# Kernel optimization log

Measured on AMD Instinct MI355X. Metric: run time of the kernel, lower is better.

Reference implementation:

```python
import jax, jax.numpy as jnp
import numpy as np

B, C, H, W = 2, 256, 64, 64
FEAT = 256          # in_channels * expansion_ratio
HEADS = 8
HS = FEAT // HEADS  # 32
OUT = 256


def setup_inputs() -> dict:
    key = jax.random.key(0)
    ks = jax.random.split(key, 12)
    inp = {
        "x": jax.random.normal(ks[0], (B, C, H, W), jnp.float32),
        "mod_multiplier": jax.random.normal(ks[1], (B, FEAT), jnp.float32),
        "mod_bias": jax.random.normal(ks[2], (B, FEAT), jnp.float32),
        # learned parameters (1x1 convs as matrices)
        "w_qkv": jax.random.normal(ks[3], (3 * FEAT, C), jnp.float32) * 0.02,
        "b_qkv": jnp.zeros((3 * FEAT,), jnp.float32),
        "w_proj": jax.random.normal(ks[4], (OUT, FEAT), jnp.float32) * 0.02,
        "pe_q_h": jax.random.normal(ks[5], (1, FEAT, H, 1), jnp.float32) * 0.02,
        "pe_q_w": jax.random.normal(ks[6], (1, FEAT, 1, W), jnp.float32) * 0.02,
        "pe_k_h": jax.random.normal(ks[7], (1, FEAT, H, 1), jnp.float32) * 0.02,
        "pe_k_w": jax.random.normal(ks[8], (1, FEAT, 1, W), jnp.float32) * 0.02,
        "pre_act_bias": jnp.zeros((1, C, 1, 1), jnp.float32),
        "pre_qkv_bias": jnp.zeros((1, C, 1, 1), jnp.float32),
        "pre_proj_bias": jnp.zeros((1, FEAT, 1, 1), jnp.float32),
        "id_scale": jnp.ones((1, OUT, 1, 1), jnp.float32),
    }
    return inp


def reference(x, mod_multiplier, mod_bias, w_qkv, b_qkv, w_proj,
              pe_q_h, pe_q_w, pe_k_h, pe_k_w,
              pre_act_bias, pre_qkv_bias, pre_proj_bias, id_scale):
    b = x.shape[0]
    # pre-activation (Fixup-style biases)
    x_preact = jax.nn.silu(x + pre_act_bias) + pre_qkv_bias
    # 1x1 conv -> QKV: [b, 3F, H, W]
    qkv = jnp.einsum('bchw,oc->bohw', x_preact, w_qkv) + b_qkv[None, :, None, None]
    q, k, v = jnp.split(qkv, 3, axis=1)
    # additive positional embeddings
    q = q + pe_q_h + pe_q_w
    k = k + pe_k_h + pe_k_w
    # FiLM modulation of query
    q = q * mod_multiplier[:, :, None, None] + mod_bias[:, :, None, None]
    # [b, heads, head_size, H*W]
    q = q.reshape(b, HEADS, HS, H * W)
    k = k.reshape(b, HEADS, HS, H * W)
    v = v.reshape(b, HEADS, HS, H * W)
    scale = jnp.asarray(HS ** 0.5, x.dtype)
    logits = jnp.einsum('bhdn,bhdm->bhnm', q, k) / scale
    weights = jax.nn.softmax(logits, axis=-1)
    attn = jnp.einsum('bhnm,bhdm->bhdn', weights, v)
    attn = attn.reshape(b, FEAT, H, W)
    # output projection (1x1 conv, no bias)
    x_res = jnp.einsum('bchw,oc->bohw', attn + pre_proj_bias, w_proj)
    return x * id_scale + x_res
```

## Files before the change

### kernel.cpp

```cpp
#include <hip/hip_runtime.h>
#include <hip/hip_bf16.h>
#include <cstdint>

#define NB   2
#define NC   256
#define NN   4096
#define NH   8
#define HSZ  32
#define NF   256
#define N3F  768

typedef __bf16 bf16x8 __attribute__((ext_vector_type(8)));
typedef __bf16 bf16x4 __attribute__((ext_vector_type(4)));
typedef short  s16x4  __attribute__((ext_vector_type(4)));
typedef float  floatx4 __attribute__((ext_vector_type(4)));

#define QSCALE 0.25506601622184f

__global__ void k_prep(const float* __restrict__ x, const float* __restrict__ pab,
                       const float* __restrict__ pqb, __bf16* __restrict__ y,
                       const float* __restrict__ wqkv, const float* __restrict__ wproj,
                       __bf16* __restrict__ wqb, __bf16* __restrict__ wpb) {
    __shared__ __bf16 ct[32 * 264];
    int bid = blockIdx.x, tid = threadIdx.x;
    if (bid >= 256) {
        int id = (bid - 256) * 1024 + tid * 4;
        const float* src = (id < 196608) ? (wqkv + id) : (wproj + (id - 196608));
        __bf16* dst = (id < 196608) ? (wqb + id) : (wpb + (id - 196608));
        float4 v = *(const float4*)src;
        bf16x4 o;
        o[0] = (__bf16)v.x; o[1] = (__bf16)v.y; o[2] = (__bf16)v.z; o[3] = (__bf16)v.w;
        *(bf16x4*)dst = o;
        return;
    }
    int b = bid >> 7, nt = bid & 127;
    int n0 = nt * 32;
    int cbase = tid >> 3, nc = tid & 7;
#pragma unroll
    for (int q = 0; q < 8; q++) {
        int c = cbase + q * 32;
        const float4 xv = *(const float4*)(x + ((size_t)b * NC + c) * NN + n0 + nc * 4);
        float bias = pab[c], qb = pqb[c];
        float vs[4] = {xv.x, xv.y, xv.z, xv.w};
#pragma unroll
        for (int i = 0; i < 4; i++) {
            float s = vs[i] + bias;
            float r = s / (1.f + __expf(-s)) + qb;
            ct[(nc * 4 + i) * 264 + c] = (__bf16)r;
        }
    }
    __syncthreads();
#pragma unroll
    for (int q = 0; q < 4; q++) {
        int id = tid + q * 256;
        int n = id >> 5, ck = (id & 31) * 8;
        bf16x8 v = *(const bf16x8*)(ct + n * 264 + ck);
        *(bf16x8*)(y + ((size_t)b * NN + n0 + n) * NC + ck) = v;
    }
}

__launch_bounds__(256)
__global__ void k_qkv(const __bf16* __restrict__ y, const __bf16* __restrict__ wb,
                      const float* __restrict__ bqkv,
                      const float* __restrict__ peqh, const float* __restrict__ peqw,
                      const float* __restrict__ pekh, const float* __restrict__ pekw,
                      const float* __restrict__ mm, const float* __restrict__ mb,
                      __bf16* __restrict__ qs, __bf16* __restrict__ kst, __bf16* __restrict__ vdm) {
    __shared__ __bf16 smem[4 * 5120];
    __bf16* at0 = smem;
    __bf16* bt0 = smem + 2 * 5120;
    __bf16* ct  = smem;
    const int nt = blockIdx.x, ot = blockIdx.y, b = blockIdx.z;
    const int tid = threadIdx.x;
    const int wave = tid >> 6, lane = tid & 63, ln = lane & 15, quad = lane >> 4;
    const int wm = (wave & 1) * 64, wn = (wave >> 1) * 64;
    floatx4 acc[4][4];
#pragma unroll
    for (int i = 0; i < 4; i++)
#pragma unroll
        for (int j = 0; j < 4; j++) acc[i][j] = 0.f;
    const __bf16* ysrc = y + ((size_t)b * NN + nt * 128) * NC;
    const __bf16* wsrc = wb + (size_t)ot * 128 * NC;
    const int r0 = tid >> 2, c0 = (tid & 3) * 8;
    const int r1 = (tid + 256) >> 2, c1 = ((tid + 256) & 3) * 8;
    bf16x8 ya0, ya1, wa0, wa1;
    ya0 = *(const bf16x8*)(ysrc + (size_t)r0 * NC + c0);
    ya1 = *(const bf16x8*)(ysrc + (size_t)r1 * NC + c1);
    wa0 = *(const bf16x8*)(wsrc + (size_t)r0 * NC + c0);
    wa1 = *(const bf16x8*)(wsrc + (size_t)r1 * NC + c1);
    for (int ko = 0; ko < 8; ko++) {
        int buf = ko & 1;
        *(bf16x8*)(at0 + buf * 5120 + r0 * 40 + c0) = ya0;
        *(bf16x8*)(at0 + buf * 5120 + r1 * 40 + c1) = ya1;
        *(bf16x8*)(bt0 + buf * 5120 + r0 * 40 + c0) = wa0;
        *(bf16x8*)(bt0 + buf * 5120 + r1 * 40 + c1) = wa1;
        __syncthreads();
        if (ko < 7) {
            int kc = (ko + 1) * 32;
            ya0 = *(const bf16x8*)(ysrc + (size_t)r0 * NC + kc + c0);
            ya1 = *(const bf16x8*)(ysrc + (size_t)r1 * NC + kc + c1);
            wa0 = *(const bf16x8*)(wsrc + (size_t)r0 * NC + kc + c0);
            wa1 = *(const bf16x8*)(wsrc + (size_t)r1 * NC + kc + c1);
        }
        const __bf16* atb = at0 + buf * 5120;
        const __bf16* btb = bt0 + buf * 5120;
        bf16x8 af[4], bfr[4];
#pragma unroll
        for (int ii = 0; ii < 4; ii++) af[ii]  = *(const bf16x8*)(atb + (wm + ii * 16 + ln) * 40 + quad * 8);
#pragma unroll
        for (int jj = 0; jj < 4; jj++) bfr[jj] = *(const bf16x8*)(btb + (wn + jj * 16 + ln) * 40 + quad * 8);
#pragma unroll
        for (int ii = 0; ii < 4; ii++)
#pragma unroll
            for (int jj = 0; jj < 4; jj++)
                acc[ii][jj] = __builtin_amdgcn_mfma_f32_16x16x32_bf16(af[ii], bfr[jj], acc[ii][jj], 0, 0, 0);
    }
    __syncthreads();
    if (ot < 4) {
#pragma unroll
        for (int ii = 0; ii < 4; ii++)
#pragma unroll
            for (int jj = 0; jj < 4; jj++) {
                int o_l = wn + jj * 16 + ln;
                int o_g = ot * 128 + o_l;
#pragma unroll
                for (int r = 0; r < 4; r++) {
                    int n_l = wm + ii * 16 + quad * 4 + r;
                    int n_g = nt * 128 + n_l;
                    int hp = n_g >> 6, wp = n_g & 63;
                    float val = acc[ii][jj][r] + bqkv[o_g];
                    if (ot < 2) {
                        val += peqh[o_g * 64 + hp] + peqw[o_g * 64 + wp];
                        val = val * mm[b * NF + o_g] + mb[b * NF + o_g];
                        val *= QSCALE;
                    } else {
                        int c = o_g - 256;
                        val += pekh[c * 64 + hp] + pekw[c * 64 + wp];
                    }
                    ct[n_l * 136 + o_l] = (__bf16)val;
                }
            }
        __syncthreads();
#pragma unroll
        for (int q = 0; q < 8; q++) {
            int id = tid + q * 256;
            int n_l = id >> 4, oc = (id & 15) * 8;
            bf16x8 v = *(const bf16x8*)(ct + n_l * 136 + oc);
            int n_g = nt * 128 + n_l;
            int o_g = ot * 128 + oc;
            if (ot < 2) {
                int h = o_g >> 5, d = o_g & 31;
                *(bf16x8*)(qs + (((size_t)b * NH + h) * NN + n_g) * HSZ + d) = v;
            } else {
                int c = o_g - 256, h = c >> 5, d = c & 31;
                *(bf16x8*)(kst + (((size_t)b * NH + h) * NN + n_g) * HSZ + d) = v;
            }
        }
    } else {
#pragma unroll
        for (int ii = 0; ii < 4; ii++)
#pragma unroll
            for (int jj = 0; jj < 4; jj++) {
                int o_l = wn + jj * 16 + ln;
                int o_g = ot * 128 + o_l;
#pragma unroll
                for (int r = 0; r < 4; r++) {
                    int n_l = wm + ii * 16 + quad * 4 + r;
                    float val = acc[ii][jj][r] + bqkv[o_g];
                    ct[o_l * 136 + n_l] = (__bf16)val;
                }
            }
        __syncthreads();
#pragma unroll
        for (int q = 0; q < 8; q++) {
            int id = tid + q * 256;
            int o_l = id >> 4, ncnk = (id & 15) * 8;
            bf16x8 v = *(const bf16x8*)(ct + o_l * 136 + ncnk);
            int c = ot * 128 + o_l - 512, h = c >> 5, d = c & 31;
            *(bf16x8*)(vdm + (((size_t)b * NH + h) * HSZ + d) * NN + nt * 128 + ncnk) = v;
        }
    }
}

__launch_bounds__(256)
__global__ void k_attn(const __bf16* __restrict__ qs, const __bf16* __restrict__ ksrc,
                       const __bf16* __restrict__ vdm,
                       __bf16* __restrict__ po, float* __restrict__ pl) {
    __shared__ __bf16 kt[2][128 * 40];
    __shared__ __bf16 vt[2][32 * 136];
    int bi = blockIdx.x;
    int xcd = bi & 7, r = bi >> 3;
    int bh = xcd * 2 + (r & 1);
    int r2 = r >> 1;
    int qt = r2 & 31, half = r2 >> 5;
    int m_base = half * 2048;
    int tid = threadIdx.x, wave = tid >> 6, lane = tid & 63, ln = lane & 15, quad = lane >> 4;
    int n0 = qt * 128 + wave * 32;
    const __bf16* qbase = qs + (size_t)bh * NN * HSZ;
    const __bf16* kbase = ksrc + (size_t)bh * NN * HSZ;
    const __bf16* vbase = vdm + (size_t)bh * HSZ * NN;
    bf16x8 qa[2];
    qa[0] = *(const bf16x8*)(qbase + (size_t)(n0 + ln) * HSZ + quad * 8);
    qa[1] = *(const bf16x8*)(qbase + (size_t)(n0 + 16 + ln) * HSZ + quad * 8);
    floatx4 o[2][2];
    o[0][0] = 0.f; o[0][1] = 0.f; o[1][0] = 0.f; o[1][1] = 0.f;
    floatx4 lsum4[2];
    lsum4[0] = 0.f; lsum4[1] = 0.f;
    floatx4 zf = 0.f;
    const int k0r = tid >> 2, k0c = (tid & 3) * 8;
    const int k1r = (tid + 256) >> 2, k1c = ((tid + 256) & 3) * 8;
    const int v0d = tid >> 4, v0m = (tid & 15) * 8;
    const int v1d = (tid + 256) >> 4, v1m = ((tid + 256) & 15) * 8;
    bf16x8 krg0, krg1, vrg0, vrg1;
    krg0 = *(const bf16x8*)(kbase + (size_t)(m_base + k0r) * HSZ + k0c);
    krg1 = *(const bf16x8*)(kbase + (size_t)(m_base + k1r) * HSZ + k1c);
    vrg0 = *(const bf16x8*)(vbase + (size_t)v0d * NN + m_base + v0m);
    vrg1 = *(const bf16x8*)(vbase + (size_t)v1d * NN + m_base + v1m);

    for (int mt = 0; mt < 16; mt++) {
        int buf = mt & 1;
        *(bf16x8*)(&kt[buf][k0r * 40 + k0c]) = krg0;
        *(bf16x8*)(&kt[buf][k1r * 40 + k1c]) = krg1;
        *(bf16x8*)(&vt[buf][v0d * 136 + v0m]) = vrg0;
        *(bf16x8*)(&vt[buf][v1d * 136 + v1m]) = vrg1;
        __syncthreads();
        if (mt < 15) {
            int m1 = m_base + (mt + 1) * 128;
            krg0 = *(const bf16x8*)(kbase + (size_t)(m1 + k0r) * HSZ + k0c);
            krg1 = *(const bf16x8*)(kbase + (size_t)(m1 + k1r) * HSZ + k1c);
            vrg0 = *(const bf16x8*)(vbase + (size_t)v0d * NN + m1 + v0m);
            vrg1 = *(const bf16x8*)(vbase + (size_t)v1d * NN + m1 + v1m);
        }
        const __bf16* ktb = &kt[buf][0];
        const __bf16* vtb = &vt[buf][0];
#pragma unroll
        for (int j = 0; j < 8; j++) {
            bf16x8 kb = *(const bf16x8*)(ktb + (j * 16 + ln) * 40 + quad * 8);
            s16x4 vb0, vb1;
            __builtin_memcpy(&vb0, vtb + ln * 136 + j * 16 + quad * 4, 8);
            __builtin_memcpy(&vb1, vtb + (16 + ln) * 136 + j * 16 + quad * 4, 8);
#pragma unroll
            for (int i = 0; i < 2; i++) {
                floatx4 s = __builtin_amdgcn_mfma_f32_16x16x32_bf16(kb, qa[i], zf, 0, 0, 0);
                bf16x4 p;
#pragma unroll
                for (int rr = 0; rr < 4; rr++) {
                    float e = __builtin_amdgcn_exp2f(s[rr]);
                    lsum4[i][rr] += e;
                    p[rr] = (__bf16)e;
                }
                s16x4 pa;
                __builtin_memcpy(&pa, &p, 8);
                o[i][0] = __builtin_amdgcn_mfma_f32_16x16x16bf16_1k(pa, vb0, o[i][0], 0, 0, 0);
                o[i][1] = __builtin_amdgcn_mfma_f32_16x16x16bf16_1k(pa, vb1, o[i][1], 0, 0, 0);
            }
        }
    }
    size_t pobase = (size_t)(half * 16 + bh) * NN * HSZ;
    size_t plbase = (size_t)(half * 16 + bh) * NN;
#pragma unroll
    for (int i = 0; i < 2; i++) {
        float ls = lsum4[i][0] + lsum4[i][1] + lsum4[i][2] + lsum4[i][3];
        ls += __shfl_xor(ls, 16, 64);
        ls += __shfl_xor(ls, 32, 64);
        if (quad == 0) pl[plbase + n0 + i * 16 + ln] = ls;
#pragma unroll
        for (int rr = 0; rr < 4; rr++) {
            int n_g = n0 + i * 16 + quad * 4 + rr;
#pragma unroll
            for (int dj = 0; dj < 2; dj++)
                po[pobase + (size_t)n_g * HSZ + dj * 16 + ln] = (__bf16)o[i][dj][rr];
        }
    }
}

__launch_bounds__(256)
__global__ void k_proj(const __bf16* __restrict__ po, const float* __restrict__ pl,
                       const __bf16* __restrict__ wpb, const float* __restrict__ ppb,
                       const float* __restrict__ x, const float* __restrict__ idsc,
                       float* __restrict__ out) {
    __shared__ __bf16 at[64 * 264];
    __shared__ __bf16 bt[2][128 * 40];
    __shared__ float linv[8 * 128];
    __shared__ float ppbs[256];
    int nt = blockIdx.x, ot = blockIdx.y, b = blockIdx.z;
    int tid = threadIdx.x, wave = tid >> 6, lane = tid & 63, ln = lane & 15, quad = lane >> 4;
    int wo = (wave & 1) * 32, wn = (wave >> 1) * 64;
#pragma unroll
    for (int q = 0; q < 8; q++) {
        int id = tid + q * 256;
        int row = id >> 5, fc = (id & 31) * 8;
        *(bf16x8*)(at + row * 264 + fc) = *(const bf16x8*)(wpb + (size_t)(ot * 64 + row) * NF + fc);
    }
#pragma unroll
    for (int q = 0; q < 4; q++) {
        int id = tid + q * 256;
        int h = id >> 7, n_l = id & 127;
        size_t base = (size_t)(b * NH + h) * NN + nt * 128 + n_l;
        linv[id] = 1.f / (pl[base] + pl[base + (size_t)16 * NN]);
    }
    ppbs[tid] = ppb[tid];
    __syncthreads();
    floatx4 acc[2][4];
#pragma unroll
    for (int i = 0; i < 2; i++)
#pragma unroll
        for (int j = 0; j < 4; j++) acc[i][j] = 0.f;
    const int n_l = tid >> 1, dh = (tid & 1) * 16;
    const size_t prow = ((size_t)b * NH * NN + (size_t)nt * 128 + n_l) * HSZ + dh;
    const size_t hstep = (size_t)NN * HSZ;
    const size_t half_off = (size_t)16 * NN * HSZ;
    bf16x8 p0a, p0b, p1a, p1b;
    p0a = *(const bf16x8*)(po + prow);
    p0b = *(const bf16x8*)(po + prow + 8);
    p1a = *(const bf16x8*)(po + prow + half_off);
    p1b = *(const bf16x8*)(po + prow + half_off + 8);
    for (int ko = 0; ko < 8; ko++) {
        int buf = ko & 1;
        float iv = linv[ko * 128 + n_l];
        bf16x8 c0, c1;
#pragma unroll
        for (int e = 0; e < 8; e++) {
            float v0 = ((float)p0a[e] + (float)p1a[e]) * iv + ppbs[ko * 32 + dh + e];
            float v1 = ((float)p0b[e] + (float)p1b[e]) * iv + ppbs[ko * 32 + dh + 8 + e];
            c0[e] = (__bf16)v0;
            c1[e] = (__bf16)v1;
        }
        *(bf16x8*)(&bt[buf][n_l * 40 + dh]) = c0;
        *(bf16x8*)(&bt[buf][n_l * 40 + dh + 8]) = c1;
        __syncthreads();
        if (ko < 7) {
            size_t pr = prow + (size_t)(ko + 1) * hstep;
            p0a = *(const bf16x8*)(po + pr);
            p0b = *(const bf16x8*)(po + pr + 8);
            p1a = *(const bf16x8*)(po + pr + half_off);
            p1b = *(const bf16x8*)(po + pr + half_off + 8);
        }
        bf16x8 af[2], bfr[4];
#pragma unroll
        for (int oi = 0; oi < 2; oi++) af[oi]  = *(const bf16x8*)(at + (wo + oi * 16 + ln) * 264 + ko * 32 + quad * 8);
#pragma unroll
        for (int nj = 0; nj < 4; nj++) bfr[nj] = *(const bf16x8*)(&bt[buf][(wn + nj * 16 + ln) * 40 + quad * 8]);
#pragma unroll
        for (int oi = 0; oi < 2; oi++)
#pragma unroll
            for (int nj = 0; nj < 4; nj++)
                acc[oi][nj] = __builtin_amdgcn_mfma_f32_16x16x32_bf16(af[oi], bfr[nj], acc[oi][nj], 0, 0, 0);
    }
#pragma unroll
    for (int oi = 0; oi < 2; oi++)
#pragma unroll
        for (int nj = 0; nj < 4; nj++)
#pragma unroll
            for (int r = 0; r < 4; r++) {
                int o_g = ot * 64 + wo + oi * 16 + quad * 4 + r;
                int n_g = nt * 128 + wn + nj * 16 + ln;
                size_t idx = ((size_t)b * NF + o_g) * NN + n_g;
                out[idx] = x[idx] * idsc[o_g] + acc[oi][nj][r];
            }
}

extern "C" void kernel_launch(void* const* d_in, const int* in_sizes, int n_in,
                              void* d_out, int out_size, void* d_ws, size_t ws_size,
                              hipStream_t stream) {
    (void)in_sizes; (void)n_in; (void)out_size; (void)ws_size;
    const float* x    = (const float*)d_in[0];
    const float* mm   = (const float*)d_in[1];
    const float* mb   = (const float*)d_in[2];
    const float* wqkv = (const float*)d_in[3];
    const float* bqkv = (const float*)d_in[4];
    const float* wproj= (const float*)d_in[5];
    const float* peqh = (const float*)d_in[6];
    const float* peqw = (const float*)d_in[7];
    const float* pekh = (const float*)d_in[8];
    const float* pekw = (const float*)d_in[9];
    const float* pab  = (const float*)d_in[10];
    const float* pqb  = (const float*)d_in[11];
    const float* ppb  = (const float*)d_in[12];
    const float* idsc = (const float*)d_in[13];
    float* out = (float*)d_out;

    __bf16* ws = (__bf16*)d_ws;
    const size_t SEG = 2097152;
    __bf16* y    = ws;
    __bf16* qs   = ws + SEG;
    __bf16* kst  = ws + SEG * 2;
    __bf16* vdm  = ws + SEG * 3;
    __bf16* po   = ws + SEG * 4;
    float*  pl   = (float*)(ws + SEG * 6);
    __bf16* wqb  = ws + SEG * 6 + 262144;
    __bf16* wpb  = wqb + 196608;

    hipLaunchKernelGGL(k_prep, dim3(512), dim3(256), 0, stream,
                       x, pab, pqb, y, wqkv, wproj, wqb, wpb);
    hipLaunchKernelGGL(k_qkv,  dim3(32, 6, 2), dim3(256), 0, stream,
                       y, wqb, bqkv, peqh, peqw, pekh, pekw, mm, mb, qs, kst, vdm);
    hipLaunchKernelGGL(k_attn, dim3(1024), dim3(256), 0, stream, qs, kst, vdm, po, pl);
    hipLaunchKernelGGL(k_proj, dim3(32, 4, 2), dim3(256), 0, stream,
                       po, pl, wpb, ppb, x, idsc, out);
}
```

Measured before the change: 198.4 us.

## Pre-swizzle K/V into MFMA fragment layout and shrink QKV/proj tiles

The QKV kernel now writes K and V directly in per-16-key MFMA fragment order, so the attention kernel stages them into LDS with flat contiguous copies and reads each fragment with a single vector load instead of padded strided accesses. The softmax row sum is now computed with an extra MFMA against a ones vector rather than per-lane adds and shuffles. The attention output is staged through LDS for coalesced vector stores. The QKV and projection kernels use 64x64 tiles, doubling the grid to improve occupancy at the cost of less data reuse per block.

```diff
diff --git a/kernel.cpp b/kernel.cpp
--- a/kernel.cpp
+++ b/kernel.cpp
@@ -65,212 +65,206 @@
                       const float* __restrict__ peqh, const float* __restrict__ peqw,
                       const float* __restrict__ pekh, const float* __restrict__ pekw,
                       const float* __restrict__ mm, const float* __restrict__ mb,
-                      __bf16* __restrict__ qs, __bf16* __restrict__ kst, __bf16* __restrict__ vdm) {
-    __shared__ __bf16 smem[4 * 5120];
-    __bf16* at0 = smem;
-    __bf16* bt0 = smem + 2 * 5120;
-    __bf16* ct  = smem;
+                      __bf16* __restrict__ qs, __bf16* __restrict__ kf, __bf16* __restrict__ vf) {
+    __shared__ __bf16 smem[4][64 * 40];
+    __bf16* ct = &smem[0][0];
     const int nt = blockIdx.x, ot = blockIdx.y, b = blockIdx.z;
     const int tid = threadIdx.x;
     const int wave = tid >> 6, lane = tid & 63, ln = lane & 15, quad = lane >> 4;
-    const int wm = (wave & 1) * 64, wn = (wave >> 1) * 64;
-    floatx4 acc[4][4];
-#pragma unroll
-    for (int i = 0; i < 4; i++)
-#pragma unroll
-        for (int j = 0; j < 4; j++) acc[i][j] = 0.f;
-    const __bf16* ysrc = y + ((size_t)b * NN + nt * 128) * NC;
-    const __bf16* wsrc = wb + (size_t)ot * 128 * NC;
+    const int wm = (wave & 1) * 32, wn = (wave >> 1) * 32;
+    floatx4 acc[2][2];
+#pragma unroll
+    for (int i = 0; i < 2; i++)
+#pragma unroll
+        for (int j = 0; j < 2; j++) acc[i][j] = 0.f;
+    const __bf16* ysrc = y + ((size_t)b * NN + nt * 64) * NC;
+    const __bf16* wsrc = wb + (size_t)ot * 64 * NC;
     const int r0 = tid >> 2, c0 = (tid & 3) * 8;
-    const int r1 = (tid + 256) >> 2, c1 = ((tid + 256) & 3) * 8;
-    bf16x8 ya0, ya1, wa0, wa1;
-    ya0 = *(const bf16x8*)(ysrc + (size_t)r0 * NC + c0);
-    ya1 = *(const bf16x8*)(ysrc + (size_t)r1 * NC + c1);
-    wa0 = *(const bf16x8*)(wsrc + (size_t)r0 * NC + c0);
-    wa1 = *(const bf16x8*)(wsrc + (size_t)r1 * NC + c1);
+    bf16x8 ya = *(const bf16x8*)(ysrc + (size_t)r0 * NC + c0);
+    bf16x8 wa = *(const bf16x8*)(wsrc + (size_t)r0 * NC + c0);
     for (int ko = 0; ko < 8; ko++) {
         int buf = ko & 1;
-        *(bf16x8*)(at0 + buf * 5120 + r0 * 40 + c0) = ya0;
-        *(bf16x8*)(at0 + buf * 5120 + r1 * 40 + c1) = ya1;
-        *(bf16x8*)(bt0 + buf * 5120 + r0 * 40 + c0) = wa0;
-        *(bf16x8*)(bt0 + buf * 5120 + r1 * 40 + c1) = wa1;
+        *(bf16x8*)(&smem[buf][r0 * 40 + c0]) = ya;
+        *(bf16x8*)(&smem[2 + buf][r0 * 40 + c0]) = wa;
         __syncthreads();
         if (ko < 7) {
             int kc = (ko + 1) * 32;
-            ya0 = *(const bf16x8*)(ysrc + (size_t)r0 * NC + kc + c0);
-            ya1 = *(const bf16x8*)(ysrc + (size_t)r1 * NC + kc + c1);
-            wa0 = *(const bf16x8*)(wsrc + (size_t)r0 * NC + kc + c0);
-            wa1 = *(const bf16x8*)(wsrc + (size_t)r1 * NC + kc + c1);
-        }
-        const __bf16* atb = at0 + buf * 5120;
-        const __bf16* btb = bt0 + buf * 5120;
-        bf16x8 af[4], bfr[4];
-#pragma unroll
-        for (int ii = 0; ii < 4; ii++) af[ii]  = *(const bf16x8*)(atb + (wm + ii * 16 + ln) * 40 + quad * 8);
-#pragma unroll
-        for (int jj = 0; jj < 4; jj++) bfr[jj] = *(const bf16x8*)(btb + (wn + jj * 16 + ln) * 40 + quad * 8);
-#pragma unroll
-        for (int ii = 0; ii < 4; ii++)
-#pragma unroll
-            for (int jj = 0; jj < 4; jj++)
+            ya = *(const bf16x8*)(ysrc + (size_t)r0 * NC + kc + c0);
+            wa = *(const bf16x8*)(wsrc + (size_t)r0 * NC + kc + c0);
+        }
+        bf16x8 af[2], bfr[2];
+#pragma unroll
+        for (int ii = 0; ii < 2; ii++) af[ii]  = *(const bf16x8*)(&smem[buf][(wm + ii * 16 + ln) * 40 + quad * 8]);
+#pragma unroll
+        for (int jj = 0; jj < 2; jj++) bfr[jj] = *(const bf16x8*)(&smem[2 + buf][(wn + jj * 16 + ln) * 40 + quad * 8]);
+#pragma unroll
+        for (int ii = 0; ii < 2; ii++)
+#pragma unroll
+            for (int jj = 0; jj < 2; jj++)
                 acc[ii][jj] = __builtin_amdgcn_mfma_f32_16x16x32_bf16(af[ii], bfr[jj], acc[ii][jj], 0, 0, 0);
     }
     __syncthreads();
-    if (ot < 4) {
-#pragma unroll
-        for (int ii = 0; ii < 4; ii++)
-#pragma unroll
-            for (int jj = 0; jj < 4; jj++) {
+    if (ot < 8) {
+#pragma unroll
+        for (int ii = 0; ii < 2; ii++)
+#pragma unroll
+            for (int jj = 0; jj < 2; jj++) {
                 int o_l = wn + jj * 16 + ln;
-                int o_g = ot * 128 + o_l;
+                int o_g = ot * 64 + o_l;
+                float bq = bqkv[o_g];
 #pragma unroll
                 for (int r = 0; r < 4; r++) {
                     int n_l = wm + ii * 16 + quad * 4 + r;
-                    int n_g = nt * 128 + n_l;
-                    int hp = n_g >> 6, wp = n_g & 63;
-                    float val = acc[ii][jj][r] + bqkv[o_g];
-                    if (ot < 2) {
-                        val += peqh[o_g * 64 + hp] + peqw[o_g * 64 + wp];
+                    float val = acc[ii][jj][r] + bq;
+                    if (ot < 4) {
+                        val += peqh[o_g * 64 + nt] + peqw[o_g * 64 + n_l];
                         val = val * mm[b * NF + o_g] + mb[b * NF + o_g];
                         val *= QSCALE;
                     } else {
                         int c = o_g - 256;
-                        val += pekh[c * 64 + hp] + pekw[c * 64 + wp];
+                        val += pekh[c * 64 + nt] + pekw[c * 64 + n_l];
                     }
-                    ct[n_l * 136 + o_l] = (__bf16)val;
+                    ct[n_l * 72 + o_l] = (__bf16)val;
                 }
             }
         __syncthreads();
 #pragma unroll
-        for (int q = 0; q < 8; q++) {
+        for (int q = 0; q < 2; q++) {
             int id = tid + q * 256;
-            int n_l = id >> 4, oc = (id & 15) * 8;
-            bf16x8 v = *(const bf16x8*)(ct + n_l * 136 + oc);
-            int n_g = nt * 128 + n_l;
-            int o_g = ot * 128 + oc;
-            if (ot < 2) {
+            int n_l = id >> 3, oc = (id & 7) * 8;
+            bf16x8 v = *(const bf16x8*)(ct + n_l * 72 + oc);
+            int n_g = nt * 64 + n_l;
+            int o_g = ot * 64 + oc;
+            if (ot < 4) {
                 int h = o_g >> 5, d = o_g & 31;
                 *(bf16x8*)(qs + (((size_t)b * NH + h) * NN + n_g) * HSZ + d) = v;
             } else {
-                int c = o_g - 256, h = c >> 5, d = c & 31;
-                *(bf16x8*)(kst + (((size_t)b * NH + h) * NN + n_g) * HSZ + d) = v;
+                int c = o_g - 256, h = c >> 5, d0 = c & 31;
+                size_t blk = ((size_t)(b * NH + h) * 256 + (n_g >> 4)) * 512;
+                *(bf16x8*)(kf + blk + (d0 >> 3) * 128 + (n_g & 15) * 8) = v;
             }
         }
     } else {
 #pragma unroll
-        for (int ii = 0; ii < 4; ii++)
-#pragma unroll
-            for (int jj = 0; jj < 4; jj++) {
+        for (int ii = 0; ii < 2; ii++)
+#pragma unroll
+            for (int jj = 0; jj < 2; jj++) {
                 int o_l = wn + jj * 16 + ln;
-                int o_g = ot * 128 + o_l;
+                float bq = bqkv[ot * 64 + o_l];
 #pragma unroll
                 for (int r = 0; r < 4; r++) {
                     int n_l = wm + ii * 16 + quad * 4 + r;
-                    float val = acc[ii][jj][r] + bqkv[o_g];
-                    ct[o_l * 136 + n_l] = (__bf16)val;
+                    ct[o_l * 72 + n_l] = (__bf16)(acc[ii][jj][r] + bq);
                 }
             }
         __syncthreads();
 #pragma unroll
-        for (int q = 0; q < 8; q++) {
+        for (int q = 0; q < 4; q++) {
             int id = tid + q * 256;
-            int o_l = id >> 4, ncnk = (id & 15) * 8;
-            bf16x8 v = *(const bf16x8*)(ct + o_l * 136 + ncnk);
-            int c = ot * 128 + o_l - 512, h = c >> 5, d = c & 31;
-            *(bf16x8*)(vdm + (((size_t)b * NH + h) * HSZ + d) * NN + nt * 128 + ncnk) = v;
+            int o_l = id >> 4, ng4 = (id & 15) * 4;
+            bf16x4 v = *(const bf16x4*)(ct + o_l * 72 + ng4);
+            int c = (ot - 8) * 64 + o_l, h = c >> 5, d = c & 31;
+            int dj = d >> 4, lnv = d & 15;
+            int m_g = nt * 64 + ng4;
+            size_t blk = ((size_t)(b * NH + h) * 256 + (m_g >> 4)) * 512;
+            *(bf16x4*)(vf + blk + (((m_g >> 2) & 3) * 16 + lnv) * 8 + dj * 4) = v;
         }
     }
 }
 
 __launch_bounds__(256)
-__global__ void k_attn(const __bf16* __restrict__ qs, const __bf16* __restrict__ ksrc,
-                       const __bf16* __restrict__ vdm,
+__global__ void k_attn(const __bf16* __restrict__ qs, const __bf16* __restrict__ kf,
+                       const __bf16* __restrict__ vf,
                        __bf16* __restrict__ po, float* __restrict__ pl) {
-    __shared__ __bf16 kt[2][128 * 40];
-    __shared__ __bf16 vt[2][32 * 136];
+    __shared__ __bf16 sbuf[2 * 8192];
     int bi = blockIdx.x;
     int xcd = bi & 7, r = bi >> 3;
     int bh = xcd * 2 + (r & 1);
     int r2 = r >> 1;
     int qt = r2 & 31, half = r2 >> 5;
-    int m_base = half * 2048;
     int tid = threadIdx.x, wave = tid >> 6, lane = tid & 63, ln = lane & 15, quad = lane >> 4;
     int n0 = qt * 128 + wave * 32;
     const __bf16* qbase = qs + (size_t)bh * NN * HSZ;
-    const __bf16* kbase = ksrc + (size_t)bh * NN * HSZ;
-    const __bf16* vbase = vdm + (size_t)bh * HSZ * NN;
+    const __bf16* kfb = kf + ((size_t)bh * 256 + half * 128) * 512;
+    const __bf16* vfb = vf + ((size_t)bh * 256 + half * 128) * 512;
     bf16x8 qa[2];
     qa[0] = *(const bf16x8*)(qbase + (size_t)(n0 + ln) * HSZ + quad * 8);
     qa[1] = *(const bf16x8*)(qbase + (size_t)(n0 + 16 + ln) * HSZ + quad * 8);
-    floatx4 o[2][2];
+    floatx4 o[2][2], o2[2];
     o[0][0] = 0.f; o[0][1] = 0.f; o[1][0] = 0.f; o[1][1] = 0.f;
-    floatx4 lsum4[2];
-    lsum4[0] = 0.f; lsum4[1] = 0.f;
+    o2[0] = 0.f; o2[1] = 0.f;
     floatx4 zf = 0.f;
-    const int k0r = tid >> 2, k0c = (tid & 3) * 8;
-    const int k1r = (tid + 256) >> 2, k1c = ((tid + 256) & 3) * 8;
-    const int v0d = tid >> 4, v0m = (tid & 15) * 8;
-    const int v1d = (tid + 256) >> 4, v1m = ((tid + 256) & 15) * 8;
-    bf16x8 krg0, krg1, vrg0, vrg1;
-    krg0 = *(const bf16x8*)(kbase + (size_t)(m_base + k0r) * HSZ + k0c);
-    krg1 = *(const bf16x8*)(kbase + (size_t)(m_base + k1r) * HSZ + k1c);
-    vrg0 = *(const bf16x8*)(vbase + (size_t)v0d * NN + m_base + v0m);
-    vrg1 = *(const bf16x8*)(vbase + (size_t)v1d * NN + m_base + v1m);
-
+    s16x4 ones;
+    ones[0] = (short)0x3F80; ones[1] = (short)0x3F80;
+    ones[2] = (short)0x3F80; ones[3] = (short)0x3F80;
+    const int toff = tid * 8;
+    const int lo = lane * 8;
+    bf16x8 kr0, kr1, vr0, vr1;
+    kr0 = *(const bf16x8*)(kfb + toff);
+    kr1 = *(const bf16x8*)(kfb + toff + 2048);
+    vr0 = *(const bf16x8*)(vfb + toff);
+    vr1 = *(const bf16x8*)(vfb + toff + 2048);
     for (int mt = 0; mt < 16; mt++) {
-        int buf = mt & 1;
-        *(bf16x8*)(&kt[buf][k0r * 40 + k0c]) = krg0;
-        *(bf16x8*)(&kt[buf][k1r * 40 + k1c]) = krg1;
-        *(bf16x8*)(&vt[buf][v0d * 136 + v0m]) = vrg0;
-        *(bf16x8*)(&vt[buf][v1d * 136 + v1m]) = vrg1;
+        int bo = (mt & 1) << 13;
+        *(bf16x8*)(sbuf + bo + toff) = kr0;
+        *(bf16x8*)(sbuf + bo + toff + 2048) = kr1;
+        *(bf16x8*)(sbuf + bo + 4096 + toff) = vr0;
+        *(bf16x8*)(sbuf + bo + 4096 + toff + 2048) = vr1;
         __syncthreads();
         if (mt < 15) {
-            int m1 = m_base + (mt + 1) * 128;
-            krg0 = *(const bf16x8*)(kbase + (size_t)(m1 + k0r) * HSZ + k0c);
-            krg1 = *(const bf16x8*)(kbase + (size_t)(m1 + k1r) * HSZ + k1c);
-            vrg0 = *(const bf16x8*)(vbase + (size_t)v0d * NN + m1 + v0m);
-            vrg1 = *(const bf16x8*)(vbase + (size_t)v1d * NN + m1 + v1m);
-        }
-        const __bf16* ktb = &kt[buf][0];
-        const __bf16* vtb = &vt[buf][0];
+            const __bf16* kn = kfb + (mt + 1) * 4096;
+            const __bf16* vn = vfb + (mt + 1) * 4096;
+            kr0 = *(const bf16x8*)(kn + toff);
+            kr1 = *(const bf16x8*)(kn + toff + 2048);
+            vr0 = *(const bf16x8*)(vn + toff);
+            vr1 = *(const bf16x8*)(vn + toff + 2048);
+        }
+        const __bf16* kl = sbuf + bo;
+        const __bf16* vl = sbuf + bo + 4096;
 #pragma unroll
         for (int j = 0; j < 8; j++) {
-            bf16x8 kb = *(const bf16x8*)(ktb + (j * 16 + ln) * 40 + quad * 8);
+            bf16x8 kfr = *(const bf16x8*)(kl + j * 512 + lo);
+            bf16x8 vfr = *(const bf16x8*)(vl + j * 512 + lo);
             s16x4 vb0, vb1;
-            __builtin_memcpy(&vb0, vtb + ln * 136 + j * 16 + quad * 4, 8);
-            __builtin_memcpy(&vb1, vtb + (16 + ln) * 136 + j * 16 + quad * 4, 8);
+            __builtin_memcpy(&vb0, &vfr, 8);
+            __builtin_memcpy(&vb1, (const char*)&vfr + 8, 8);
 #pragma unroll
             for (int i = 0; i < 2; i++) {
-                floatx4 s = __builtin_amdgcn_mfma_f32_16x16x32_bf16(kb, qa[i], zf, 0, 0, 0);
+                floatx4 s = __builtin_amdgcn_mfma_f32_16x16x32_bf16(kfr, qa[i], zf, 0, 0, 0);
                 bf16x4 p;
 #pragma unroll
-                for (int rr = 0; rr < 4; rr++) {
-                    float e = __builtin_amdgcn_exp2f(s[rr]);
-                    lsum4[i][rr] += e;
-                    p[rr] = (__bf16)e;
-                }
+                for (int rr = 0; rr < 4; rr++)
+                    p[rr] = (__bf16)__builtin_amdgcn_exp2f(s[rr]);
                 s16x4 pa;
                 __builtin_memcpy(&pa, &p, 8);
                 o[i][0] = __builtin_amdgcn_mfma_f32_16x16x16bf16_1k(pa, vb0, o[i][0], 0, 0, 0);
                 o[i][1] = __builtin_amdgcn_mfma_f32_16x16x16bf16_1k(pa, vb1, o[i][1], 0, 0, 0);
-            }
-        }
-    }
-    size_t pobase = (size_t)(half * 16 + bh) * NN * HSZ;
+                o2[i]   = __builtin_amdgcn_mfma_f32_16x16x16bf16_1k(pa, ones, o2[i], 0, 0, 0);
+            }
+        }
+    }
     size_t plbase = (size_t)(half * 16 + bh) * NN;
-#pragma unroll
-    for (int i = 0; i < 2; i++) {
-        float ls = lsum4[i][0] + lsum4[i][1] + lsum4[i][2] + lsum4[i][3];
-        ls += __shfl_xor(ls, 16, 64);
-        ls += __shfl_xor(ls, 32, 64);
-        if (quad == 0) pl[plbase + n0 + i * 16 + ln] = ls;
-#pragma unroll
-        for (int rr = 0; rr < 4; rr++) {
-            int n_g = n0 + i * 16 + quad * 4 + rr;
-#pragma unroll
-            for (int dj = 0; dj < 2; dj++)
-                po[pobase + (size_t)n_g * HSZ + dj * 16 + ln] = (__bf16)o[i][dj][rr];
-        }
+    if (ln == 0)
+#pragma unroll
+        for (int i = 0; i < 2; i++)
+#pragma unroll
+            for (int rr = 0; rr < 4; rr++)
+                pl[plbase + n0 + i * 16 + quad * 4 + rr] = o2[i][rr];
+    __bf16* ct = sbuf;
+#pragma unroll
+    for (int i = 0; i < 2; i++)
+#pragma unroll
+        for (int dj = 0; dj < 2; dj++)
+#pragma unroll
+            for (int rr = 0; rr < 4; rr++)
+                ct[(wave * 32 + i * 16 + quad * 4 + rr) * 32 + dj * 16 + ln] = (__bf16)o[i][dj][rr];
+    __syncthreads();
+    size_t pobase = ((size_t)(half * 16 + bh) * NN + (size_t)qt * 128) * HSZ;
+#pragma unroll
+    for (int q = 0; q < 2; q++) {
+        int id = tid + q * 256;
+        int n_l = id >> 2, dc = (id & 3) * 8;
+        *(bf16x8*)(po + pobase + n_l * HSZ + dc) = *(const bf16x8*)(ct + n_l * 32 + dc);
     }
 }
 
@@ -280,12 +274,12 @@
                        const float* __restrict__ x, const float* __restrict__ idsc,
                        float* __restrict__ out) {
     __shared__ __bf16 at[64 * 264];
-    __shared__ __bf16 bt[2][128 * 40];
-    __shared__ float linv[8 * 128];
+    __shared__ __bf16 bt[2][64 * 40];
+    __shared__ float linv[8 * 64];
     __shared__ float ppbs[256];
     int nt = blockIdx.x, ot = blockIdx.y, b = blockIdx.z;
     int tid = threadIdx.x, wave = tid >> 6, lane = tid & 63, ln = lane & 15, quad = lane >> 4;
-    int wo = (wave & 1) * 32, wn = (wave >> 1) * 64;
+    int wo = (wave & 1) * 32, wn = (wave >> 1) * 32;
 #pragma unroll
     for (int q = 0; q < 8; q++) {
         int id = tid + q * 256;
@@ -293,68 +287,58 @@
         *(bf16x8*)(at + row * 264 + fc) = *(const bf16x8*)(wpb + (size_t)(ot * 64 + row) * NF + fc);
     }
 #pragma unroll
-    for (int q = 0; q < 4; q++) {
+    for (int q = 0; q < 2; q++) {
         int id = tid + q * 256;
-        int h = id >> 7, n_l = id & 127;
-        size_t base = (size_t)(b * NH + h) * NN + nt * 128 + n_l;
+        int h = id >> 6, n_l = id & 63;
+        size_t base = (size_t)(b * NH + h) * NN + nt * 64 + n_l;
         linv[id] = 1.f / (pl[base] + pl[base + (size_t)16 * NN]);
     }
     ppbs[tid] = ppb[tid];
     __syncthreads();
-    floatx4 acc[2][4];
+    floatx4 acc[2][2];
 #pragma unroll
     for (int i = 0; i < 2; i++)
 #pragma unroll
-        for (int j = 0; j < 4; j++) acc[i][j] = 0.f;
-    const int n_l = tid >> 1, dh = (tid & 1) * 16;
-    const size_t prow = ((size_t)b * NH * NN + (size_t)nt * 128 + n_l) * HSZ + dh;
+        for (int j = 0; j < 2; j++) acc[i][j] = 0.f;
+    const int n_l = tid >> 2, dh8 = (tid & 3) * 8;
     const size_t hstep = (size_t)NN * HSZ;
     const size_t half_off = (size_t)16 * NN * HSZ;
-    bf16x8 p0a, p0b, p1a, p1b;
-    p0a = *(const bf16x8*)(po + prow);
-    p0b = *(const bf16x8*)(po + prow + 8);
-    p1a = *(const bf16x8*)(po + prow + half_off);
-    p1b = *(const bf16x8*)(po + prow + half_off + 8);
+    size_t prow = ((size_t)b * NH * NN + (size_t)nt * 64 + n_l) * HSZ + dh8;
+    bf16x8 p0 = *(const bf16x8*)(po + prow);
+    bf16x8 p1 = *(const bf16x8*)(po + prow + half_off);
     for (int ko = 0; ko < 8; ko++) {
         int buf = ko & 1;
-        float iv = linv[ko * 128 + n_l];
-        bf16x8 c0, c1;
-#pragma unroll
-        for (int e = 0; e < 8; e++) {
-            float v0 = ((float)p0a[e] + (float)p1a[e]) * iv + ppbs[ko * 32 + dh + e];
-            float v1 = ((float)p0b[e] + (float)p1b[e]) * iv + ppbs[ko * 32 + dh + 8 + e];
-            c0[e] = (__bf16)v0;
-            c1[e] = (__bf16)v1;
-        }
-        *(bf16x8*)(&bt[buf][n_l * 40 + dh]) = c0;
-        *(bf16x8*)(&bt[buf][n_l * 40 + dh + 8]) = c1;
+        float iv = linv[ko * 64 + n_l];
+        bf16x8 c;
+#pragma unroll
+        for (int e = 0; e < 8; e++)
+            c[e] = (__bf16)(((float)p0[e] + (float)p1[e]) * iv + ppbs[ko * 32 + dh8 + e]);
+        *(bf16x8*)(&bt[buf][n_l * 40 + dh8]) = c;
         __syncthreads();
         if (ko < 7) {
             size_t pr = prow + (size_t)(ko + 1) * hstep;
-            p0a = *(const bf16x8*)(po + pr);
-            p0b = *(const bf16x8*)(po + pr + 8);
-            p1a = *(const bf16x8*)(po + pr + half_off);
-            p1b = *(const bf16x8*)(po + pr + half_off + 8);
-        }
-        bf16x8 af[2], bfr[4];
+            p0 = *(const bf16x8*)(po + pr);
+            p1 = *(const bf16x8*)(po + pr + half_off);
+        }
+        bf16x8 af[2], bfr[2];
 #pragma unroll
         for (int oi = 0; oi < 2; oi++) af[oi]  = *(const bf16x8*)(at + (wo + oi * 16 + ln) * 264 + ko * 32 + quad * 8);
 #pragma unroll
-        for (int nj = 0; nj < 4; nj++) bfr[nj] = *(const bf16x8*)(&bt[buf][(wn + nj * 16 + ln) * 40 + quad * 8]);
+        for (int nj = 0; nj < 2; nj++) bfr[nj] = *(const bf16x8*)(&bt[buf][(wn + nj * 16 + ln) * 40 + quad * 8]);
 #pragma unroll
         for (int oi = 0; oi < 2; oi++)
 #pragma unroll
-            for (int nj = 0; nj < 4; nj++)
+            for (int nj = 0; nj < 2; nj++)
                 acc[oi][nj] = __builtin_amdgcn_mfma_f32_16x16x32_bf16(af[oi], bfr[nj], acc[oi][nj], 0, 0, 0);
     }
 #pragma unroll
     for (int oi = 0; oi < 2; oi++)
 #pragma unroll
-        for (int nj = 0; nj < 4; nj++)
+        for (int nj = 0; nj < 2; nj++)
 #pragma unroll
             for (int r = 0; r < 4; r++) {
                 int o_g = ot * 64 + wo + oi * 16 + quad * 4 + r;
-                int n_g = nt * 128 + wn + nj * 16 + ln;
+                int n_g = nt * 64 + wn + nj * 16 + ln;
                 size_t idx = ((size_t)b * NF + o_g) * NN + n_g;
                 out[idx] = x[idx] * idsc[o_g] + acc[oi][nj][r];
             }
@@ -384,8 +368,8 @@
     const size_t SEG = 2097152;
     __bf16* y    = ws;
     __bf16* qs   = ws + SEG;
-    __bf16* kst  = ws + SEG * 2;
-    __bf16* vdm  = ws + SEG * 3;
+    __bf16* kf   = ws + SEG * 2;
+    __bf16* vf   = ws + SEG * 3;
     __bf16* po   = ws + SEG * 4;
     float*  pl   = (float*)(ws + SEG * 6);
     __bf16* wqb  = ws + SEG * 6 + 262144;
@@ -393,9 +377,9 @@
 
     hipLaunchKernelGGL(k_prep, dim3(512), dim3(256), 0, stream,
                        x, pab, pqb, y, wqkv, wproj, wqb, wpb);
-    hipLaunchKernelGGL(k_qkv,  dim3(32, 6, 2), dim3(256), 0, stream,
-                       y, wqb, bqkv, peqh, peqw, pekh, pekw, mm, mb, qs, kst, vdm);
-    hipLaunchKernelGGL(k_attn, dim3(1024), dim3(256), 0, stream, qs, kst, vdm, po, pl);
-    hipLaunchKernelGGL(k_proj, dim3(32, 4, 2), dim3(256), 0, stream,
+    hipLaunchKernelGGL(k_qkv,  dim3(64, 12, 2), dim3(256), 0, stream,
+                       y, wqb, bqkv, peqh, peqw, pekh, pekw, mm, mb, qs, kf, vf);
+    hipLaunchKernelGGL(k_attn, dim3(1024), dim3(256), 0, stream, qs, kf, vf, po, pl);
+    hipLaunchKernelGGL(k_proj, dim3(64, 4, 2), dim3(256), 0, stream,
                        po, pl, wpb, ppb, x, idsc, out);
 }
```

Result: faster. 175.0 us (-11.8%).
